# Kernel tuning notes

Hardware: AMD Instinct MI355X
Metric: run time of the kernel (lower is better)

## Reference

```python
import jax, jax.numpy as jnp
import numpy as np

B = 8192        # batch
DB = 64         # dim_body
DO = 128        # dim_object
NOBJ = 9        # nb_objects (all connected)
NE = 72         # edges = NOBJ*(NOBJ-1)
DE = 128        # edge feature dim
NISO = 3        # isolated nodes
HID = 256
PHI_OUT = 256
ACT = 32
LOG_SIG_MIN, LOG_SIG_MAX = -20.0, 2.0


def setup_inputs() -> dict:
    key = jax.random.key(0)
    ks = jax.random.split(key, 16)
    s = 0.05
    return {
        "obs": jax.random.normal(ks[0], (B, DB + NOBJ * DO), jnp.float32),
        "edge_features": jax.random.normal(ks[1], (B, NE, DE), jnp.float32),
        # every object id 0..8 appears NE//NOBJ times (static edge targets)
        "edges_to": jnp.tile(jnp.arange(NOBJ, dtype=jnp.int32), NE // NOBJ),
        "isolated_nodes": jax.random.normal(ks[2], (B, NISO, DO), jnp.float32),
        "isolated_nodes_features": jax.random.normal(ks[3], (B, NISO, DE), jnp.float32),
        "W1_phi": jax.random.normal(ks[4], (DB + DO + DE, HID), jnp.float32) * s,
        "b1_phi": jnp.zeros((HID,), jnp.float32),
        "W2_phi": jax.random.normal(ks[5], (HID, PHI_OUT), jnp.float32) * s,
        "b2_phi": jnp.zeros((PHI_OUT,), jnp.float32),
        "W1_rho": jax.random.normal(ks[6], (PHI_OUT, HID), jnp.float32) * s,
        "b1_rho": jnp.zeros((HID,), jnp.float32),
        "Wm": jax.random.normal(ks[7], (HID, ACT), jnp.float32) * s,
        "bm": jnp.zeros((ACT,), jnp.float32),
        "Ws": jax.random.normal(ks[8], (HID, ACT), jnp.float32) * s,
        "bs": jnp.zeros((ACT,), jnp.float32),
    }


def reference(obs, edge_features, edges_to, isolated_nodes, isolated_nodes_features,
              W1_phi, b1_phi, W2_phi, b2_phi, W1_rho, b1_rho, Wm, bm, Ws, bs):
    obs_body = obs[:, :DB]                              # [B, DB]
    obs_objects = obs[:, DB:].reshape(B, NOBJ, DO)      # [B, NOBJ, DO]

    # per-node max over incoming edges (segment-max over static edge targets)
    ef = jnp.transpose(edge_features, (1, 0, 2))        # [NE, B, DE]
    incoming = jax.ops.segment_max(ef, edges_to, num_segments=NOBJ)  # [NOBJ, B, DE]

    body_c = jnp.broadcast_to(obs_body, (NOBJ, B, DB))
    inp_connected = jnp.concatenate(
        [body_c, jnp.transpose(obs_objects, (1, 0, 2)), incoming], axis=-1)

    body_i = jnp.broadcast_to(obs_body, (NISO, B, DB))
    inp_isolated = jnp.concatenate(
        [body_i,
         jnp.transpose(isolated_nodes, (1, 0, 2)),
         jnp.transpose(isolated_nodes_features, (1, 0, 2))], axis=-1)

    inp = jnp.concatenate([inp_connected, inp_isolated], axis=0)  # [NOBJ+NISO, B, DB+DO+DE]

    # phi DeepSet MLP
    h = jax.nn.relu(inp @ W1_phi + b1_phi)
    phi = jax.nn.relu(h @ W2_phi + b2_phi)

    pooled = phi.sum(axis=0)                            # readout='sum' -> [B, PHI_OUT]

    # rho MLP -> (mean, log_std)
    r = jax.nn.relu(pooled @ W1_rho + b1_rho)
    mean = r @ Wm + bm
    log_std = jnp.clip(r @ Ws + bs, LOG_SIG_MIN, LOG_SIG_MAX)
    return mean, log_std
```

## Files before the change

kernel.cpp:

```cpp
#include <hip/hip_runtime.h>
#include <hip/hip_bf16.h>
#include <stdint.h>


#define Bsz   8192
#define OBSW  1216
#define NH    256

typedef unsigned short u16;
typedef unsigned int   u32;

using bf16x8 = __attribute__((ext_vector_type(8))) short;
using f32x4  = __attribute__((ext_vector_type(4))) float;

__device__ __attribute__((aligned(16))) u16 g_W1t[256 * 320];
__device__ __attribute__((aligned(16))) u16 g_W2t[256 * 256];
__device__ __attribute__((aligned(16))) u16 g_Rt [256 * 256];
__device__ __attribute__((aligned(16))) u16 g_Wcat[64 * 256];

__device__ __forceinline__ u16 f2bf(float f) {
  union { float f; u32 i; } v; v.f = f;
  u32 x = v.i;
  x += 0x7fffu + ((x >> 16) & 1u);
  return (u16)(x >> 16);
}
__device__ __forceinline__ ushort4 pack4(float4 f) {
  ushort4 o = { f2bf(f.x), f2bf(f.y), f2bf(f.z), f2bf(f.w) };
  return o;
}

__global__ __launch_bounds__(256)
void transpose_all(const float* __restrict__ W1, const float* __restrict__ W2,
                   const float* __restrict__ Wr, const float* __restrict__ Wm,
                   const float* __restrict__ Wsg) {
  __shared__ u16 tile[32][33];
  int bx = blockIdx.x;
  const float* in; u16* out; int K, N, row_off = 0, k0, n0;
  if (bx < 80)       { in = W1;  out = g_W1t;  K = 320; N = 256; k0 = (bx % 10) * 32; n0 = (bx / 10) * 32; }
  else if (bx < 144) { bx -= 80;  in = W2;  out = g_W2t;  K = 256; N = 256; k0 = (bx & 7) * 32; n0 = (bx >> 3) * 32; }
  else if (bx < 208) { bx -= 144; in = Wr;  out = g_Rt;   K = 256; N = 256; k0 = (bx & 7) * 32; n0 = (bx >> 3) * 32; }
  else if (bx < 216) { bx -= 208; in = Wm;  out = g_Wcat; K = 256; N = 32;  k0 = bx * 32; n0 = 0; }
  else               { bx -= 216; in = Wsg; out = g_Wcat; K = 256; N = 32;  k0 = bx * 32; n0 = 0; row_off = 32; }
  int c = threadIdx.x & 31, r0 = threadIdx.x >> 5;
  #pragma unroll
  for (int i = 0; i < 4; i++) {
    int r = r0 + i * 8;
    tile[r][c] = f2bf(in[(size_t)(k0 + r) * N + (n0 + c)]);
  }
  __syncthreads();
  #pragma unroll
  for (int i = 0; i < 4; i++) {
    int r = r0 + i * 8;
    out[(size_t)(n0 + r + row_off) * K + (k0 + c)] = tile[c][r];
  }
}

__global__ __launch_bounds__(512, 2)
void node_kernel(const float* __restrict__ obs, const float* __restrict__ ef,
                 const float* __restrict__ iso, const float* __restrict__ isof,
                 const float* __restrict__ b1, const float* __restrict__ b2,
                 const float* __restrict__ br, const float* __restrict__ bm,
                 const float* __restrict__ bs, float* __restrict__ out) {
  __shared__ __attribute__((aligned(16))) u16 As[16][328];
  __shared__ __attribute__((aligned(16))) u16 Ht[16][264];
  const int b0 = blockIdx.x * 16;
  const int tid = threadIdx.x;
  const int wave = tid >> 6, lane = tid & 63;
  const int w32 = wave * 32, lrow = lane & 15, quad = lane >> 4;
  const int sr = tid >> 5, sc = tid & 31, dq4 = sc * 4;
  const size_t ar = (size_t)(b0 + sr);

  bf16x8 w1f[10][2];
  #pragma unroll
  for (int kc = 0; kc < 10; kc++)
    #pragma unroll
    for (int nb = 0; nb < 2; nb++)
      w1f[kc][nb] = *(const bf16x8*)(g_W1t + (size_t)(w32 + nb * 16 + lrow) * 320
                                     + kc * 32 + quad * 8);
  bf16x8 w2f[8][2];
  #pragma unroll
  for (int kc = 0; kc < 8; kc++)
    #pragma unroll
    for (int nb = 0; nb < 2; nb++)
      w2f[kc][nb] = *(const bf16x8*)(g_W2t + (size_t)(w32 + nb * 16 + lrow) * 256
                                     + kc * 32 + quad * 8);

  float bv1[2], bv2[2];
  #pragma unroll
  for (int nb = 0; nb < 2; nb++) {
    int col = w32 + nb * 16 + lrow;
    bv1[nb] = b1[col]; bv2[nb] = b2[col];
  }

  {
    if (sc < 16) {
      float4 fb = *(const float4*)(obs + ar * OBSW + dq4);
      *(ushort4*)(&As[sr][dq4]) = pack4(fb);
    }
    float4 pa = *(const float4*)(obs + ar * OBSW + 64 + dq4);
    const float* base = ef + (ar * 72 + 0) * 128 + dq4;
    float4 m = *(const float4*)base;
    #pragma unroll
    for (int j = 1; j < 8; j++) {
      float4 w = *(const float4*)(base + (size_t)j * 1152);
      m.x = fmaxf(m.x, w.x); m.y = fmaxf(m.y, w.y);
      m.z = fmaxf(m.z, w.z); m.w = fmaxf(m.w, w.w);
    }
    *(ushort4*)(&As[sr][64  + dq4]) = pack4(pa);
    *(ushort4*)(&As[sr][192 + dq4]) = pack4(m);
  }
  __syncthreads();

  const f32x4 vzero = {0.f, 0.f, 0.f, 0.f};
  f32x4 pool[2] = {vzero, vzero};

  for (int n = 0; n < 12; n++) {
    const int n1 = n + 1;
    float4 pe[8]; float4 pa; float4 ps;
    if (n1 < 12) {
      if (n1 < 9) {
        pa = *(const float4*)(obs + ar * OBSW + 64 + (size_t)n1 * 128 + dq4);
        const float* base = ef + (ar * 72 + n1) * 128 + dq4;
        #pragma unroll
        for (int j = 0; j < 8; j++)
          pe[j] = *(const float4*)(base + (size_t)j * 1152);
      } else {
        pa = *(const float4*)(iso  + (ar * 3 + (n1 - 9)) * 128 + dq4);
        ps = *(const float4*)(isof + (ar * 3 + (n1 - 9)) * 128 + dq4);
      }
    }

    f32x4 acc[2] = {vzero, vzero};
    #pragma unroll
    for (int kc = 0; kc < 10; kc++) {
      bf16x8 af = *(const bf16x8*)(&As[lrow][kc * 32 + quad * 8]);
      #pragma unroll
      for (int nb = 0; nb < 2; nb++)
        acc[nb] = __builtin_amdgcn_mfma_f32_16x16x32_bf16(af, w1f[kc][nb],
                                                          acc[nb], 0, 0, 0);
    }
    #pragma unroll
    for (int nb = 0; nb < 2; nb++) {
      int col = w32 + nb * 16 + lrow;
      #pragma unroll
      for (int i = 0; i < 4; i++)
        Ht[quad * 4 + i][col] = f2bf(fmaxf(acc[nb][i] + bv1[nb], 0.f));
    }
    __syncthreads();

    if (n1 < 12) {
      *(ushort4*)(&As[sr][64 + dq4]) = pack4(pa);
      if (n1 < 9) {
        float4 m = pe[0];
        #pragma unroll
        for (int j = 1; j < 8; j++) {
          m.x = fmaxf(m.x, pe[j].x); m.y = fmaxf(m.y, pe[j].y);
          m.z = fmaxf(m.z, pe[j].z); m.w = fmaxf(m.w, pe[j].w);
        }
        *(ushort4*)(&As[sr][192 + dq4]) = pack4(m);
      } else {
        *(ushort4*)(&As[sr][192 + dq4]) = pack4(ps);
      }
    }

    f32x4 acc2[2] = {vzero, vzero};
    #pragma unroll
    for (int kc = 0; kc < 8; kc++) {
      bf16x8 af = *(const bf16x8*)(&Ht[lrow][kc * 32 + quad * 8]);
      #pragma unroll
      for (int nb = 0; nb < 2; nb++)
        acc2[nb] = __builtin_amdgcn_mfma_f32_16x16x32_bf16(af, w2f[kc][nb],
                                                           acc2[nb], 0, 0, 0);
    }
    #pragma unroll
    for (int nb = 0; nb < 2; nb++)
      #pragma unroll
      for (int i = 0; i < 4; i++)
        pool[nb][i] += fmaxf(acc2[nb][i] + bv2[nb], 0.f);
    __syncthreads();
  }

  #pragma unroll
  for (int nb = 0; nb < 2; nb++) {
    int col = w32 + nb * 16 + lrow;
    #pragma unroll
    for (int i = 0; i < 4; i++)
      Ht[quad * 4 + i][col] = f2bf(pool[nb][i]);
  }
  __syncthreads();

  f32x4 acc3[2] = {vzero, vzero};
  #pragma unroll
  for (int kc = 0; kc < 8; kc++) {
    bf16x8 af = *(const bf16x8*)(&Ht[lrow][kc * 32 + quad * 8]);
    #pragma unroll
    for (int nb = 0; nb < 2; nb++) {
      bf16x8 bq = *(const bf16x8*)(g_Rt + (size_t)(w32 + nb * 16 + lrow) * 256
                                   + kc * 32 + quad * 8);
      acc3[nb] = __builtin_amdgcn_mfma_f32_16x16x32_bf16(af, bq, acc3[nb], 0, 0, 0);
    }
  }
  __syncthreads();
  #pragma unroll
  for (int nb = 0; nb < 2; nb++) {
    int col = w32 + nb * 16 + lrow;
    float bv = br[col];
    #pragma unroll
    for (int i = 0; i < 4; i++)
      Ht[quad * 4 + i][col] = f2bf(fmaxf(acc3[nb][i] + bv, 0.f));
  }
  __syncthreads();

  if (wave < 4) {
    f32x4 acch = vzero;
    #pragma unroll
    for (int kc = 0; kc < 8; kc++) {
      bf16x8 af = *(const bf16x8*)(&Ht[lrow][kc * 32 + quad * 8]);
      bf16x8 bq = *(const bf16x8*)(g_Wcat + (size_t)(wave * 16 + lrow) * 256
                                   + kc * 32 + quad * 8);
      acch = __builtin_amdgcn_mfma_f32_16x16x32_bf16(af, bq, acch, 0, 0, 0);
    }
    int j = wave * 16 + lrow;
    #pragma unroll
    for (int i = 0; i < 4; i++) {
      int b = b0 + quad * 4 + i;
      if (j < 32) {
        out[(size_t)b * 32 + j] = acch[i] + bm[j];
      } else {
        float v = acch[i] + bs[j - 32];
        v = fminf(fmaxf(v, -20.f), 2.f);
        out[(size_t)Bsz * 32 + (size_t)b * 32 + (j - 32)] = v;
      }
    }
  }
}

extern "C" void kernel_launch(void* const* d_in, const int* in_sizes, int n_in,
                              void* d_out, int out_size, void* d_ws, size_t ws_size,
                              hipStream_t stream) {
  const float* obs  = (const float*)d_in[0];
  const float* ef   = (const float*)d_in[1];
  const float* iso  = (const float*)d_in[3];
  const float* isof = (const float*)d_in[4];
  const float* W1   = (const float*)d_in[5];
  const float* b1   = (const float*)d_in[6];
  const float* W2   = (const float*)d_in[7];
  const float* b2   = (const float*)d_in[8];
  const float* Wr   = (const float*)d_in[9];
  const float* br   = (const float*)d_in[10];
  const float* Wm   = (const float*)d_in[11];
  const float* bm   = (const float*)d_in[12];
  const float* Wsg  = (const float*)d_in[13];
  const float* bs   = (const float*)d_in[14];
  float* out = (float*)d_out;
  (void)d_ws; (void)ws_size;

  transpose_all<<<224, 256, 0, stream>>>(W1, W2, Wr, Wm, Wsg);
  node_kernel<<<Bsz / 16, 512, 0, stream>>>(obs, ef, iso, isof,
                                            b1, b2, br, bm, bs, out);
}
```

Before: 490.3 us.

## Deepen input prefetch to two nodes ahead and stream W2 fragments from global

Replaces the one-node-ahead register prefetch with a double-buffered two-node-ahead scheme, alternating two prefetch structs across an unrolled pair of iterations, to hide more global-load latency for the edge-feature max. To make room in registers, the W2 weight fragments are no longer held in VGPRs but reloaded from global (L1/L2-cached) inside each second-layer GEMM. The edge max reduction is also rewritten as a balanced tree. The cost is extra per-iteration global loads for W2 and a possible rise in register pressure from two in-flight prefetch buffers.

```diff
diff --git a/kernel.cpp b/kernel.cpp
--- a/kernel.cpp
+++ b/kernel.cpp
@@ -28,6 +28,8 @@
   ushort4 o = { f2bf(f.x), f2bf(f.y), f2bf(f.z), f2bf(f.w) };
   return o;
 }
+
+struct PF { float4 pe[8]; float4 pa; float4 ps; };
 
 __global__ __launch_bounds__(256)
 void transpose_all(const float* __restrict__ W1, const float* __restrict__ W2,
@@ -52,6 +54,46 @@
   for (int i = 0; i < 4; i++) {
     int r = r0 + i * 8;
     out[(size_t)(n0 + r + row_off) * K + (k0 + c)] = tile[c][r];
+  }
+}
+
+__device__ __forceinline__ void issueL(int n2, size_t ar, int dq4,
+    const float* __restrict__ obs, const float* __restrict__ ef,
+    const float* __restrict__ iso, const float* __restrict__ isof, PF& d) {
+  if (n2 < 9) {
+    d.pa = *(const float4*)(obs + ar * OBSW + 64 + (size_t)n2 * 128 + dq4);
+    const float* base = ef + (ar * 72 + n2) * 128 + dq4;
+    #pragma unroll
+    for (int j = 0; j < 8; j++)
+      d.pe[j] = *(const float4*)(base + (size_t)j * 1152);
+  } else {
+    d.pa = *(const float4*)(iso  + (ar * 3 + (n2 - 9)) * 128 + dq4);
+    d.ps = *(const float4*)(isof + (ar * 3 + (n2 - 9)) * 128 + dq4);
+  }
+}
+
+__device__ __forceinline__ void stageA(int n1, int sr, int dq4, PF& c,
+                                       u16 (*As)[328]) {
+  *(ushort4*)(&As[sr][64 + dq4]) = pack4(c.pa);
+  if (n1 < 9) {
+    float4 m01, m23, m45, m67, ma, mb, m;
+    m01.x = fmaxf(c.pe[0].x, c.pe[1].x); m01.y = fmaxf(c.pe[0].y, c.pe[1].y);
+    m01.z = fmaxf(c.pe[0].z, c.pe[1].z); m01.w = fmaxf(c.pe[0].w, c.pe[1].w);
+    m23.x = fmaxf(c.pe[2].x, c.pe[3].x); m23.y = fmaxf(c.pe[2].y, c.pe[3].y);
+    m23.z = fmaxf(c.pe[2].z, c.pe[3].z); m23.w = fmaxf(c.pe[2].w, c.pe[3].w);
+    m45.x = fmaxf(c.pe[4].x, c.pe[5].x); m45.y = fmaxf(c.pe[4].y, c.pe[5].y);
+    m45.z = fmaxf(c.pe[4].z, c.pe[5].z); m45.w = fmaxf(c.pe[4].w, c.pe[5].w);
+    m67.x = fmaxf(c.pe[6].x, c.pe[7].x); m67.y = fmaxf(c.pe[6].y, c.pe[7].y);
+    m67.z = fmaxf(c.pe[6].z, c.pe[7].z); m67.w = fmaxf(c.pe[6].w, c.pe[7].w);
+    ma.x = fmaxf(m01.x, m23.x); ma.y = fmaxf(m01.y, m23.y);
+    ma.z = fmaxf(m01.z, m23.z); ma.w = fmaxf(m01.w, m23.w);
+    mb.x = fmaxf(m45.x, m67.x); mb.y = fmaxf(m45.y, m67.y);
+    mb.z = fmaxf(m45.z, m67.z); mb.w = fmaxf(m45.w, m67.w);
+    m.x = fmaxf(ma.x, mb.x); m.y = fmaxf(ma.y, mb.y);
+    m.z = fmaxf(ma.z, mb.z); m.w = fmaxf(ma.w, mb.w);
+    *(ushort4*)(&As[sr][192 + dq4]) = pack4(m);
+  } else {
+    *(ushort4*)(&As[sr][192 + dq4]) = pack4(c.ps);
   }
 }
 
@@ -77,13 +119,8 @@
     for (int nb = 0; nb < 2; nb++)
       w1f[kc][nb] = *(const bf16x8*)(g_W1t + (size_t)(w32 + nb * 16 + lrow) * 320
                                      + kc * 32 + quad * 8);
-  bf16x8 w2f[8][2];
-  #pragma unroll
-  for (int kc = 0; kc < 8; kc++)
-    #pragma unroll
-    for (int nb = 0; nb < 2; nb++)
-      w2f[kc][nb] = *(const bf16x8*)(g_W2t + (size_t)(w32 + nb * 16 + lrow) * 256
-                                     + kc * 32 + quad * 8);
+  const u16* w2r0 = g_W2t + (size_t)(w32 + lrow) * 256 + quad * 8;
+  const u16* w2r1 = g_W2t + (size_t)(w32 + 16 + lrow) * 256 + quad * 8;
 
   float bv1[2], bv2[2];
   #pragma unroll
@@ -92,43 +129,22 @@
     bv1[nb] = b1[col]; bv2[nb] = b2[col];
   }
 
-  {
-    if (sc < 16) {
-      float4 fb = *(const float4*)(obs + ar * OBSW + dq4);
-      *(ushort4*)(&As[sr][dq4]) = pack4(fb);
-    }
-    float4 pa = *(const float4*)(obs + ar * OBSW + 64 + dq4);
-    const float* base = ef + (ar * 72 + 0) * 128 + dq4;
-    float4 m = *(const float4*)base;
-    #pragma unroll
-    for (int j = 1; j < 8; j++) {
-      float4 w = *(const float4*)(base + (size_t)j * 1152);
-      m.x = fmaxf(m.x, w.x); m.y = fmaxf(m.y, w.y);
-      m.z = fmaxf(m.z, w.z); m.w = fmaxf(m.w, w.w);
-    }
-    *(ushort4*)(&As[sr][64  + dq4]) = pack4(pa);
-    *(ushort4*)(&As[sr][192 + dq4]) = pack4(m);
-  }
-  __syncthreads();
-
   const f32x4 vzero = {0.f, 0.f, 0.f, 0.f};
   f32x4 pool[2] = {vzero, vzero};
-
-  for (int n = 0; n < 12; n++) {
-    const int n1 = n + 1;
-    float4 pe[8]; float4 pa; float4 ps;
-    if (n1 < 12) {
-      if (n1 < 9) {
-        pa = *(const float4*)(obs + ar * OBSW + 64 + (size_t)n1 * 128 + dq4);
-        const float* base = ef + (ar * 72 + n1) * 128 + dq4;
-        #pragma unroll
-        for (int j = 0; j < 8; j++)
-          pe[j] = *(const float4*)(base + (size_t)j * 1152);
-      } else {
-        pa = *(const float4*)(iso  + (ar * 3 + (n1 - 9)) * 128 + dq4);
-        ps = *(const float4*)(isof + (ar * 3 + (n1 - 9)) * 128 + dq4);
-      }
-    }
+  PF pfA, pfB;
+
+  {
+    float4 fb;
+    if (sc < 16) fb = *(const float4*)(obs + ar * OBSW + dq4);
+    issueL(0, ar, dq4, obs, ef, iso, isof, pfA);
+    issueL(1, ar, dq4, obs, ef, iso, isof, pfB);
+    if (sc < 16) *(ushort4*)(&As[sr][dq4]) = pack4(fb);
+    stageA(0, sr, dq4, pfA, As);
+  }
+  __syncthreads();
+
+  auto node_iter = [&](int n, PF& cons, PF& iss) {
+    if (n + 2 < 12) issueL(n + 2, ar, dq4, obs, ef, iso, isof, iss);
 
     f32x4 acc[2] = {vzero, vzero};
     #pragma unroll
@@ -148,29 +164,16 @@
     }
     __syncthreads();
 
-    if (n1 < 12) {
-      *(ushort4*)(&As[sr][64 + dq4]) = pack4(pa);
-      if (n1 < 9) {
-        float4 m = pe[0];
-        #pragma unroll
-        for (int j = 1; j < 8; j++) {
-          m.x = fmaxf(m.x, pe[j].x); m.y = fmaxf(m.y, pe[j].y);
-          m.z = fmaxf(m.z, pe[j].z); m.w = fmaxf(m.w, pe[j].w);
-        }
-        *(ushort4*)(&As[sr][192 + dq4]) = pack4(m);
-      } else {
-        *(ushort4*)(&As[sr][192 + dq4]) = pack4(ps);
-      }
-    }
+    if (n + 1 < 12) stageA(n + 1, sr, dq4, cons, As);
 
     f32x4 acc2[2] = {vzero, vzero};
     #pragma unroll
     for (int kc = 0; kc < 8; kc++) {
-      bf16x8 af = *(const bf16x8*)(&Ht[lrow][kc * 32 + quad * 8]);
-      #pragma unroll
-      for (int nb = 0; nb < 2; nb++)
-        acc2[nb] = __builtin_amdgcn_mfma_f32_16x16x32_bf16(af, w2f[kc][nb],
-                                                           acc2[nb], 0, 0, 0);
+      bf16x8 af  = *(const bf16x8*)(&Ht[lrow][kc * 32 + quad * 8]);
+      bf16x8 bq0 = *(const bf16x8*)(w2r0 + kc * 32);
+      bf16x8 bq1 = *(const bf16x8*)(w2r1 + kc * 32);
+      acc2[0] = __builtin_amdgcn_mfma_f32_16x16x32_bf16(af, bq0, acc2[0], 0, 0, 0);
+      acc2[1] = __builtin_amdgcn_mfma_f32_16x16x32_bf16(af, bq1, acc2[1], 0, 0, 0);
     }
     #pragma unroll
     for (int nb = 0; nb < 2; nb++)
@@ -178,6 +181,11 @@
       for (int i = 0; i < 4; i++)
         pool[nb][i] += fmaxf(acc2[nb][i] + bv2[nb], 0.f);
     __syncthreads();
+  };
+
+  for (int n = 0; n < 12; n += 2) {
+    node_iter(n,     pfB, pfA);
+    node_iter(n + 1, pfA, pfB);
   }
 
   #pragma unroll
```

Measured after the change: 648.9 us. +32.4%, slower.
